# Performance work log

Measured on AMD Instinct MI355X. Metric: run time of the kernel, lower is better.

The kernel has to match this reference:

```python
import jax, jax.numpy as jnp
import numpy as np


def gcn_conv(x, edge_index, W, b):
    """PyG-style GCNConv: add self-loops, symmetric degree norm, scatter-add."""
    N = x.shape[0]
    loops = jnp.arange(N, dtype=edge_index.dtype)
    src = jnp.concatenate([edge_index[0], loops])  # message sources
    dst = jnp.concatenate([edge_index[1], loops])  # aggregation targets
    h = x @ W  # [N, out] linear transform before propagation
    deg = jax.ops.segment_sum(jnp.ones_like(dst, dtype=h.dtype), dst, num_segments=N)
    dinv = jnp.where(deg > 0, jax.lax.rsqrt(jnp.maximum(deg, 1.0)), 0.0)
    norm = dinv[src] * dinv[dst]  # [E+N]
    msgs = norm[:, None] * h[src]  # gather + scale
    out = jax.ops.segment_sum(msgs, dst, num_segments=N)  # scatter-add
    return out + b


def setup_inputs() -> dict:
    key = jax.random.key(0)
    k1, k2, k3, k4 = jax.random.split(key, 4)
    N, E, F, H, C = 100000, 3200000, 256, 32, 16
    x = jax.random.normal(k1, (N, F), dtype=jnp.float32)
    edge_index = jax.random.randint(k2, (2, E), 0, N)
    W1 = jax.random.normal(k3, (F, H), dtype=jnp.float32) * 0.05
    b1 = jnp.zeros((H,), dtype=jnp.float32)
    W2 = jax.random.normal(k4, (H, C), dtype=jnp.float32) * 0.1
    b2 = jnp.zeros((C,), dtype=jnp.float32)
    return {"x": x, "edge_index": edge_index, "W1": W1, "b1": b1, "W2": W2, "b2": b2}


def reference(x, edge_index, W1, b1, W2, b2):
    h = jax.nn.relu(gcn_conv(x, edge_index, W1, b1))
    out = gcn_conv(h, edge_index, W2, b2)
    return jax.nn.softmax(out, axis=1)
```

## Files before the change

### kernel.cpp

```cpp
#include <hip/hip_runtime.h>
#include <math.h>

constexpr int Fdim = 256;
constexpr int Hdim = 32;
constexpr int Cdim = 16;
constexpr int CAP = 88;
constexpr int EPB = 8192;
constexpr int MAXNB = 512;

__global__ __launch_bounds__(256) void k_zero_int(int* __restrict__ p, int n) {
  int i = blockIdx.x * blockDim.x + threadIdx.x;
  if (i < n) p[i] = 0;
}

__global__ __launch_bounds__(256) void k_binB(const int* __restrict__ src,
                                              const int* __restrict__ dst,
                                              int* __restrict__ bcur,
                                              unsigned* __restrict__ pairs,
                                              int e, int nb, int bcap) {
  __shared__ int hist[MAXNB];
  __shared__ int cbase[MAXNB];
  int lo = blockIdx.x * EPB;
  int hi = lo + EPB;
  if (hi > e) hi = e;
  for (int t = threadIdx.x; t < nb; t += 256) hist[t] = 0;
  __syncthreads();
  for (int i = lo + threadIdx.x; i < hi; i += 256) {
    atomicAdd(&hist[dst[i] >> 8], 1);
  }
  __syncthreads();
  for (int t = threadIdx.x; t < nb; t += 256) {
    int h = hist[t];
    int base = h ? atomicAdd(&bcur[t], h) : 0;
    cbase[t] = t * bcap + base;
    hist[t] = 0;
  }
  __syncthreads();
  for (int i = lo + threadIdx.x; i < hi; i += 256) {
    int d = dst[i];
    int bk = d >> 8;
    int o = atomicAdd(&hist[bk], 1);
    int idx = cbase[bk] + o;
    if (idx < (bk + 1) * bcap)
      pairs[idx] = ((unsigned)(d & 255) << 24) | (unsigned)src[i];
  }
}

__global__ __launch_bounds__(256) void k_binC(const int* __restrict__ bcur,
                                              const unsigned* __restrict__ pairs,
                                              int* __restrict__ csr,
                                              int* __restrict__ cntg,
                                              float* __restrict__ dinv,
                                              int n, int bcap) {
  __shared__ int cnt2[256];
  __shared__ int cur2[256];
  int b = blockIdx.x;
  int nE = bcur[b];
  if (nE > bcap) nE = bcap;
  int base = b * bcap;
  cnt2[threadIdx.x] = 0;
  __syncthreads();
  for (int i = threadIdx.x; i < nE; i += 256) {
    atomicAdd(&cnt2[pairs[base + i] >> 24], 1);
  }
  __syncthreads();
  int d = b * 256 + threadIdx.x;
  int c = cnt2[threadIdx.x];
  if (d < n) {
    cntg[d] = c;
    dinv[d] = 1.0f / sqrtf((float)(c + 1));
  }
  cur2[threadIdx.x] = 0;
  __syncthreads();
  for (int i = threadIdx.x; i < nE; i += 256) {
    unsigned w = pairs[base + i];
    int loc = (int)(w >> 24);
    int s = (int)(w & 0xFFFFFFu);
    int o = atomicAdd(&cur2[loc], 1);
    if (o < CAP) csr[(size_t)(b * 256 + loc) * CAP + o] = s;
  }
}

__global__ __launch_bounds__(256) void k_lin1(const float4* __restrict__ x4,
                                              const float* __restrict__ W,
                                              const float* __restrict__ dinv,
                                              float4* __restrict__ hs, int n) {
  int row = blockIdx.x * blockDim.x + threadIdx.x;
  if (row >= n) return;
  float acc[Hdim];
#pragma unroll
  for (int c = 0; c < Hdim; ++c) acc[c] = 0.f;
  const float4* xr = x4 + (size_t)row * (Fdim / 4);
  int phase = (blockIdx.x & 3) << 4;
#pragma unroll 1
  for (int t = 0; t < Fdim / 4; ++t) {
    int k4 = (t + phase) & (Fdim / 4 - 1);
    float4 xv = xr[k4];
    const float* wp = W + k4 * 4 * Hdim;
#pragma unroll
    for (int c = 0; c < Hdim; ++c) acc[c] = fmaf(xv.x, wp[c], acc[c]);
#pragma unroll
    for (int c = 0; c < Hdim; ++c) acc[c] = fmaf(xv.y, wp[Hdim + c], acc[c]);
#pragma unroll
    for (int c = 0; c < Hdim; ++c) acc[c] = fmaf(xv.z, wp[2 * Hdim + c], acc[c]);
#pragma unroll
    for (int c = 0; c < Hdim; ++c) acc[c] = fmaf(xv.w, wp[3 * Hdim + c], acc[c]);
  }
  float di = dinv[row];
  float4* hp = hs + (size_t)row * (Hdim / 4);
#pragma unroll
  for (int q = 0; q < Hdim / 4; ++q) {
    float4 v;
    v.x = di * acc[4 * q + 0];
    v.y = di * acc[4 * q + 1];
    v.z = di * acc[4 * q + 2];
    v.w = di * acc[4 * q + 3];
    hp[q] = v;
  }
}

__global__ __launch_bounds__(256) void k_g1l2(const int* __restrict__ cnt,
                                              const int* __restrict__ csr,
                                              const float4* __restrict__ hs,
                                              const float* __restrict__ dinv,
                                              const float* __restrict__ b1,
                                              const float* __restrict__ W2,
                                              float4* __restrict__ hs2, int n) {
  int t = blockIdx.x * blockDim.x + threadIdx.x;
  int d = t >> 3, f = t & 7;
  if (d >= n) return;
  int c = cnt[d];
  if (c > CAP) c = CAP;
  const int* row = csr + (size_t)d * CAP;
  float4 acc = hs[(size_t)d * 8 + f];
  int k = 0;
  for (; k + 1 < c; k += 2) {
    int s0 = row[k], s1 = row[k + 1];
    float4 v0 = hs[(size_t)s0 * 8 + f];
    float4 v1 = hs[(size_t)s1 * 8 + f];
    acc.x += v0.x + v1.x; acc.y += v0.y + v1.y;
    acc.z += v0.z + v1.z; acc.w += v0.w + v1.w;
  }
  if (k < c) {
    int s = row[k];
    float4 v = hs[(size_t)s * 8 + f];
    acc.x += v.x; acc.y += v.y; acc.z += v.z; acc.w += v.w;
  }
  float di = dinv[d];
  float h[4];
  h[0] = fmaxf(fmaf(di, acc.x, b1[4 * f + 0]), 0.f);
  h[1] = fmaxf(fmaf(di, acc.y, b1[4 * f + 1]), 0.f);
  h[2] = fmaxf(fmaf(di, acc.z, b1[4 * f + 2]), 0.f);
  h[3] = fmaxf(fmaf(di, acc.w, b1[4 * f + 3]), 0.f);
  float p[Cdim];
#pragma unroll
  for (int j = 0; j < Cdim; ++j) p[j] = 0.f;
#pragma unroll
  for (int r = 0; r < 4; ++r) {
    const float* w = W2 + (4 * f + r) * Cdim;
#pragma unroll
    for (int j = 0; j < Cdim; ++j) p[j] = fmaf(h[r], w[j], p[j]);
  }
#pragma unroll
  for (int m = 1; m < 8; m <<= 1) {
#pragma unroll
    for (int j = 0; j < Cdim; ++j) p[j] += __shfl_xor(p[j], m, 64);
  }
  if (f < 4) {
    float4 o;
    o.x = di * p[4 * f + 0];
    o.y = di * p[4 * f + 1];
    o.z = di * p[4 * f + 2];
    o.w = di * p[4 * f + 3];
    hs2[(size_t)d * 4 + f] = o;
  }
}

__global__ __launch_bounds__(256) void k_g2sm(const int* __restrict__ cnt,
                                              const int* __restrict__ csr,
                                              const float4* __restrict__ hs,
                                              const float* __restrict__ dinv,
                                              const float* __restrict__ b2,
                                              float4* __restrict__ out, int n) {
  int t = blockIdx.x * blockDim.x + threadIdx.x;
  int d = t >> 2, f = t & 3;
  if (d >= n) return;
  int c = cnt[d];
  if (c > CAP) c = CAP;
  const int* row = csr + (size_t)d * CAP;
  float4 acc = hs[(size_t)d * 4 + f];
  int k = 0;
  for (; k + 1 < c; k += 2) {
    int s0 = row[k], s1 = row[k + 1];
    float4 v0 = hs[(size_t)s0 * 4 + f];
    float4 v1 = hs[(size_t)s1 * 4 + f];
    acc.x += v0.x + v1.x; acc.y += v0.y + v1.y;
    acc.z += v0.z + v1.z; acc.w += v0.w + v1.w;
  }
  if (k < c) {
    int s = row[k];
    float4 v = hs[(size_t)s * 4 + f];
    acc.x += v.x; acc.y += v.y; acc.z += v.z; acc.w += v.w;
  }
  float di = dinv[d];
  float v0 = fmaf(di, acc.x, b2[4 * f + 0]);
  float v1 = fmaf(di, acc.y, b2[4 * f + 1]);
  float v2 = fmaf(di, acc.z, b2[4 * f + 2]);
  float v3 = fmaf(di, acc.w, b2[4 * f + 3]);
  float m = fmaxf(fmaxf(v0, v1), fmaxf(v2, v3));
  m = fmaxf(m, __shfl_xor(m, 1, 64));
  m = fmaxf(m, __shfl_xor(m, 2, 64));
  float e0 = expf(v0 - m), e1 = expf(v1 - m), e2 = expf(v2 - m), e3 = expf(v3 - m);
  float s = e0 + e1 + e2 + e3;
  s += __shfl_xor(s, 1, 64);
  s += __shfl_xor(s, 2, 64);
  float inv = 1.f / s;
  float4 o;
  o.x = e0 * inv; o.y = e1 * inv; o.z = e2 * inv; o.w = e3 * inv;
  out[(size_t)d * 4 + f] = o;
}

extern "C" void kernel_launch(void* const* d_in, const int* in_sizes, int n_in,
                              void* d_out, int out_size, void* d_ws, size_t ws_size,
                              hipStream_t stream) {
  const float* x = (const float*)d_in[0];
  const int* ei = (const int*)d_in[1];
  const float* W1 = (const float*)d_in[2];
  const float* b1 = (const float*)d_in[3];
  const float* W2 = (const float*)d_in[4];
  const float* b2 = (const float*)d_in[5];
  float* out = (float*)d_out;

  const int N = in_sizes[0] / Fdim;
  const int E = in_sizes[1] / 2;
  const int* srcp = ei;
  const int* dstp = ei + E;

  const int NB = (N + 255) >> 8;
  const int mean = (E + NB - 1) / NB;
  const int BCAP = mean + mean / 16 + 256;

  char* ws = (char*)d_ws;
  int* bcur = (int*)ws;      ws += (size_t)MAXNB * 4;
  float* dinv = (float*)ws;  ws += (size_t)N * 4;
  int* cntg = (int*)ws;      ws += (size_t)N * 4;
  int* csr = (int*)ws;       ws += (size_t)N * CAP * 4;
  char* region = ws;
  unsigned* pairs = (unsigned*)region;
  float* hs1 = (float*)region;
  float* hs2 = (float*)(region + (size_t)N * Hdim * 4);

  int nb_n = (N + 255) / 256;
  int nbB = (E + EPB - 1) / EPB;

  k_zero_int<<<(NB + 255) / 256, 256, 0, stream>>>(bcur, NB);
  k_binB<<<nbB, 256, 0, stream>>>(srcp, dstp, bcur, pairs, E, NB, BCAP);
  k_binC<<<NB, 256, 0, stream>>>(bcur, pairs, csr, cntg, dinv, N, BCAP);

  k_lin1<<<nb_n, 256, 0, stream>>>((const float4*)x, W1, dinv, (float4*)hs1, N);

  int nb_g1 = (N * 8 + 255) / 256;
  k_g1l2<<<nb_g1, 256, 0, stream>>>(cntg, csr, (const float4*)hs1, dinv, b1, W2,
                                    (float4*)hs2, N);

  int nb_g2 = (N * 4 + 255) / 256;
  k_g2sm<<<nb_g2, 256, 0, stream>>>(cntg, csr, (const float4*)hs2, dinv, b2,
                                    (float4*)out, N);
}
```

Before: 275.0 us.

## Replace fixed-capacity padded adjacency with compact CSR via bucket prefix scans

Swaps the padded per-node neighbor array (CAP slots per node) for a compact CSR. A new single-block scan kernel computes bucket offsets, and an in-block scan in binC computes per-row starts. The goal is a smaller csr footprint and more contiguous index reads in the gather kernels, and it drops the CAP truncation. The change also unrolls the gather loops by four, removes the phase offset in the linear layer, and splits that launch into three pieces, which adds an extra serial scan launch and more launches.

```diff
diff --git a/kernel.cpp b/kernel.cpp
--- a/kernel.cpp
+++ b/kernel.cpp
@@ -4,7 +4,6 @@
 constexpr int Fdim = 256;
 constexpr int Hdim = 32;
 constexpr int Cdim = 16;
-constexpr int CAP = 88;
 constexpr int EPB = 8192;
 constexpr int MAXNB = 512;
 
@@ -46,55 +45,91 @@
   }
 }
 
+__global__ __launch_bounds__(512) void k_scanb(const int* __restrict__ bcur,
+                                               int* __restrict__ bbase,
+                                               int nb, int bcap) {
+  __shared__ int s[512];
+  int t = threadIdx.x;
+  int v = 0;
+  if (t < nb) {
+    v = bcur[t];
+    if (v > bcap) v = bcap;
+  }
+  s[t] = v;
+  __syncthreads();
+  for (int off = 1; off < 512; off <<= 1) {
+    int u = (t >= off) ? s[t - off] : 0;
+    __syncthreads();
+    s[t] += u;
+    __syncthreads();
+  }
+  if (t < nb) bbase[t] = s[t] - v;
+}
+
 __global__ __launch_bounds__(256) void k_binC(const int* __restrict__ bcur,
+                                              const int* __restrict__ bbase,
                                               const unsigned* __restrict__ pairs,
                                               int* __restrict__ csr,
+                                              int* __restrict__ rowptr,
                                               int* __restrict__ cntg,
                                               float* __restrict__ dinv,
                                               int n, int bcap) {
   __shared__ int cnt2[256];
+  __shared__ int loc0[256];
   __shared__ int cur2[256];
   int b = blockIdx.x;
+  int tid = threadIdx.x;
   int nE = bcur[b];
   if (nE > bcap) nE = bcap;
   int base = b * bcap;
-  cnt2[threadIdx.x] = 0;
-  __syncthreads();
-  for (int i = threadIdx.x; i < nE; i += 256) {
+  cnt2[tid] = 0;
+  __syncthreads();
+  for (int i = tid; i < nE; i += 256) {
     atomicAdd(&cnt2[pairs[base + i] >> 24], 1);
   }
   __syncthreads();
-  int d = b * 256 + threadIdx.x;
-  int c = cnt2[threadIdx.x];
+  int c = cnt2[tid];
+  loc0[tid] = c;
+  __syncthreads();
+  for (int off = 1; off < 256; off <<= 1) {
+    int u = (tid >= off) ? loc0[tid - off] : 0;
+    __syncthreads();
+    loc0[tid] += u;
+    __syncthreads();
+  }
+  int rowstart = bbase[b] + loc0[tid] - c;
+  __syncthreads();
+  loc0[tid] = rowstart;
+  cur2[tid] = 0;
+  int d = b * 256 + tid;
   if (d < n) {
+    rowptr[d] = rowstart;
     cntg[d] = c;
     dinv[d] = 1.0f / sqrtf((float)(c + 1));
   }
-  cur2[threadIdx.x] = 0;
-  __syncthreads();
-  for (int i = threadIdx.x; i < nE; i += 256) {
+  __syncthreads();
+  for (int i = tid; i < nE; i += 256) {
     unsigned w = pairs[base + i];
     int loc = (int)(w >> 24);
     int s = (int)(w & 0xFFFFFFu);
     int o = atomicAdd(&cur2[loc], 1);
-    if (o < CAP) csr[(size_t)(b * 256 + loc) * CAP + o] = s;
+    csr[loc0[loc] + o] = s;
   }
 }
 
 __global__ __launch_bounds__(256) void k_lin1(const float4* __restrict__ x4,
                                               const float* __restrict__ W,
                                               const float* __restrict__ dinv,
-                                              float4* __restrict__ hs, int n) {
-  int row = blockIdx.x * blockDim.x + threadIdx.x;
+                                              float4* __restrict__ hs,
+                                              int r0, int n) {
+  int row = r0 + blockIdx.x * blockDim.x + threadIdx.x;
   if (row >= n) return;
   float acc[Hdim];
 #pragma unroll
   for (int c = 0; c < Hdim; ++c) acc[c] = 0.f;
   const float4* xr = x4 + (size_t)row * (Fdim / 4);
-  int phase = (blockIdx.x & 3) << 4;
 #pragma unroll 1
-  for (int t = 0; t < Fdim / 4; ++t) {
-    int k4 = (t + phase) & (Fdim / 4 - 1);
+  for (int k4 = 0; k4 < Fdim / 4; ++k4) {
     float4 xv = xr[k4];
     const float* wp = W + k4 * 4 * Hdim;
 #pragma unroll
@@ -119,7 +154,8 @@
   }
 }
 
-__global__ __launch_bounds__(256) void k_g1l2(const int* __restrict__ cnt,
+__global__ __launch_bounds__(256) void k_g1l2(const int* __restrict__ rowptr,
+                                              const int* __restrict__ cnt,
                                               const int* __restrict__ csr,
                                               const float4* __restrict__ hs,
                                               const float* __restrict__ dinv,
@@ -130,18 +166,21 @@
   int d = t >> 3, f = t & 7;
   if (d >= n) return;
   int c = cnt[d];
-  if (c > CAP) c = CAP;
-  const int* row = csr + (size_t)d * CAP;
+  const int* row = csr + rowptr[d];
   float4 acc = hs[(size_t)d * 8 + f];
   int k = 0;
-  for (; k + 1 < c; k += 2) {
-    int s0 = row[k], s1 = row[k + 1];
+  for (; k + 3 < c; k += 4) {
+    int s0 = row[k], s1 = row[k + 1], s2 = row[k + 2], s3 = row[k + 3];
     float4 v0 = hs[(size_t)s0 * 8 + f];
     float4 v1 = hs[(size_t)s1 * 8 + f];
-    acc.x += v0.x + v1.x; acc.y += v0.y + v1.y;
-    acc.z += v0.z + v1.z; acc.w += v0.w + v1.w;
-  }
-  if (k < c) {
+    float4 v2 = hs[(size_t)s2 * 8 + f];
+    float4 v3 = hs[(size_t)s3 * 8 + f];
+    acc.x += (v0.x + v1.x) + (v2.x + v3.x);
+    acc.y += (v0.y + v1.y) + (v2.y + v3.y);
+    acc.z += (v0.z + v1.z) + (v2.z + v3.z);
+    acc.w += (v0.w + v1.w) + (v2.w + v3.w);
+  }
+  for (; k < c; ++k) {
     int s = row[k];
     float4 v = hs[(size_t)s * 8 + f];
     acc.x += v.x; acc.y += v.y; acc.z += v.z; acc.w += v.w;
@@ -176,7 +215,8 @@
   }
 }
 
-__global__ __launch_bounds__(256) void k_g2sm(const int* __restrict__ cnt,
+__global__ __launch_bounds__(256) void k_g2sm(const int* __restrict__ rowptr,
+                                              const int* __restrict__ cnt,
                                               const int* __restrict__ csr,
                                               const float4* __restrict__ hs,
                                               const float* __restrict__ dinv,
@@ -186,18 +226,21 @@
   int d = t >> 2, f = t & 3;
   if (d >= n) return;
   int c = cnt[d];
-  if (c > CAP) c = CAP;
-  const int* row = csr + (size_t)d * CAP;
+  const int* row = csr + rowptr[d];
   float4 acc = hs[(size_t)d * 4 + f];
   int k = 0;
-  for (; k + 1 < c; k += 2) {
-    int s0 = row[k], s1 = row[k + 1];
+  for (; k + 3 < c; k += 4) {
+    int s0 = row[k], s1 = row[k + 1], s2 = row[k + 2], s3 = row[k + 3];
     float4 v0 = hs[(size_t)s0 * 4 + f];
     float4 v1 = hs[(size_t)s1 * 4 + f];
-    acc.x += v0.x + v1.x; acc.y += v0.y + v1.y;
-    acc.z += v0.z + v1.z; acc.w += v0.w + v1.w;
-  }
-  if (k < c) {
+    float4 v2 = hs[(size_t)s2 * 4 + f];
+    float4 v3 = hs[(size_t)s3 * 4 + f];
+    acc.x += (v0.x + v1.x) + (v2.x + v3.x);
+    acc.y += (v0.y + v1.y) + (v2.y + v3.y);
+    acc.z += (v0.z + v1.z) + (v2.z + v3.z);
+    acc.w += (v0.w + v1.w) + (v2.w + v3.w);
+  }
+  for (; k < c; ++k) {
     int s = row[k];
     float4 v = hs[(size_t)s * 4 + f];
     acc.x += v.x; acc.y += v.y; acc.z += v.z; acc.w += v.w;
@@ -242,28 +285,39 @@
 
   char* ws = (char*)d_ws;
   int* bcur = (int*)ws;      ws += (size_t)MAXNB * 4;
+  int* bbase = (int*)ws;     ws += (size_t)MAXNB * 4;
   float* dinv = (float*)ws;  ws += (size_t)N * 4;
   int* cntg = (int*)ws;      ws += (size_t)N * 4;
-  int* csr = (int*)ws;       ws += (size_t)N * CAP * 4;
+  int* rowptr = (int*)ws;    ws += (size_t)(N + 4) * 4;
+  int* csr = (int*)ws;       ws += (size_t)E * 4;
   char* region = ws;
   unsigned* pairs = (unsigned*)region;
   float* hs1 = (float*)region;
   float* hs2 = (float*)(region + (size_t)N * Hdim * 4);
 
-  int nb_n = (N + 255) / 256;
   int nbB = (E + EPB - 1) / EPB;
 
   k_zero_int<<<(NB + 255) / 256, 256, 0, stream>>>(bcur, NB);
   k_binB<<<nbB, 256, 0, stream>>>(srcp, dstp, bcur, pairs, E, NB, BCAP);
-  k_binC<<<NB, 256, 0, stream>>>(bcur, pairs, csr, cntg, dinv, N, BCAP);
-
-  k_lin1<<<nb_n, 256, 0, stream>>>((const float4*)x, W1, dinv, (float4*)hs1, N);
+  k_scanb<<<1, 512, 0, stream>>>(bcur, bbase, NB, BCAP);
+  k_binC<<<NB, 256, 0, stream>>>(bcur, bbase, pairs, csr, rowptr, cntg, dinv, N, BCAP);
+
+  {
+    int nb_total = (N + 255) / 256;
+    int nb1 = nb_total / 3;
+    int nb2 = nb_total / 3;
+    int nb3 = nb_total - nb1 - nb2;
+    int r1 = nb1 * 256, r2 = (nb1 + nb2) * 256;
+    k_lin1<<<nb1, 256, 0, stream>>>((const float4*)x, W1, dinv, (float4*)hs1, 0, N);
+    k_lin1<<<nb2, 256, 0, stream>>>((const float4*)x, W1, dinv, (float4*)hs1, r1, N);
+    k_lin1<<<nb3, 256, 0, stream>>>((const float4*)x, W1, dinv, (float4*)hs1, r2, N);
+  }
 
   int nb_g1 = (N * 8 + 255) / 256;
-  k_g1l2<<<nb_g1, 256, 0, stream>>>(cntg, csr, (const float4*)hs1, dinv, b1, W2,
-                                    (float4*)hs2, N);
+  k_g1l2<<<nb_g1, 256, 0, stream>>>(rowptr, cntg, csr, (const float4*)hs1, dinv,
+                                    b1, W2, (float4*)hs2, N);
 
   int nb_g2 = (N * 4 + 255) / 256;
-  k_g2sm<<<nb_g2, 256, 0, stream>>>(cntg, csr, (const float4*)hs2, dinv, b2,
-                                    (float4*)out, N);
-}
+  k_g2sm<<<nb_g2, 256, 0, stream>>>(rowptr, cntg, csr, (const float4*)hs2, dinv,
+                                    b2, (float4*)out, N);
+}
```

After: 361.9 us. 31.6% more time.
